# Kernel optimization log

Hardware: AMD Instinct MI355X
Metric: run time of the kernel (lower is better)

## Reference

```python
import jax, jax.numpy as jnp
import numpy as np

N = 8192        # total nodes in the batch of graphs
E = 262144      # edges (avg degree 32)
F_IN = 128      # input node features
G = 64          # graphs in batch
C = 10          # classes
K1, K2, K3 = 4096, 2048, 1024  # int(0.5*N), int(0.5*K1), int(0.5*K2)


def setup_inputs() -> dict:
    key = jax.random.key(0)
    ks = jax.random.split(key, 16)
    def lin(k, i, o):
        return jax.random.normal(k, (i, o), jnp.float32) / np.float32(np.sqrt(i))
    return {
        "x": jax.random.normal(ks[0], (N, F_IN), jnp.float32),
        "edge_index": jax.random.randint(ks[1], (2, E), 0, N),
        "batch": jnp.sort(jax.random.randint(ks[2], (N,), 0, G)),
        "W1": lin(ks[3], F_IN, 32), "b1": jnp.zeros((32,), jnp.float32),
        "W2": lin(ks[4], 32, 64),   "b2": jnp.zeros((64,), jnp.float32),
        "W3": lin(ks[5], 64, 128),  "b3": jnp.zeros((128,), jnp.float32),
        "W4": lin(ks[6], 128, 256), "b4": jnp.zeros((256,), jnp.float32),
        "W5": lin(ks[7], 384, 128), "b5": jnp.zeros((128,), jnp.float32),
        "W6": lin(ks[8], 192, 64),  "b6": jnp.zeros((64,), jnp.float32),
        "W7": lin(ks[9], 96, 32),   "b7": jnp.zeros((32,), jnp.float32),
        "p1": jax.random.normal(ks[10], (32,), jnp.float32),
        "p2": jax.random.normal(ks[11], (64,), jnp.float32),
        "p3": jax.random.normal(ks[12], (128,), jnp.float32),
        "Wl1": lin(ks[13], 64, 64),
        "Wc": lin(ks[14], 64, C), "bc": jnp.zeros((C,), jnp.float32),
    }


def _gcn(A, x, W, b):
    # PyG GCNConv (improved=False): out = D^-1/2 (A+I) D^-1/2 propagated src->dst.
    n = A.shape[0]
    Ah = A + jnp.eye(n, dtype=A.dtype)
    deg = Ah.sum(axis=0)                                  # degree at targets (cols)
    dinv = jnp.where(deg > 0, deg ** -0.5, 0.0).astype(A.dtype)
    An = dinv[:, None] * Ah * dinv[None, :]               # edge norm d[src]^-.5 * d[dst]^-.5
    return An.T @ (x @ W) + b                             # out[dst] += norm * (xW)[src]


def _gpool(A, x, p, k):
    # GPool: scores = Linear(x)/||p||, top-k select, gate by sigmoid, reindex dense adj.
    scores = (x @ p) / jnp.linalg.norm(p)                 # [n]
    vals, idx = jax.lax.top_k(scores, k)
    xp = x[idx] * jax.nn.sigmoid(vals)[:, None]
    Ap = (A[idx][:, idx] > 0).astype(x.dtype)             # dense_to_sparse rebinarizes
    return xp, Ap, idx


def reference(x, edge_index, batch, W1, b1, W2, b2, W3, b3, W4, b4, W5, b5,
              W6, b6, W7, b7, p1, p2, p3, Wl1, Wc, bc):
    elu = jax.nn.elu
    # to_dense_adj: dense N x N adjacency (duplicate edges accumulate)
    A = jnp.zeros((N, N), x.dtype).at[edge_index[0], edge_index[1]].add(1.0)
    x1 = elu(_gcn(A, x, W1, b1))
    x2, A2, i2 = _gpool(A, x1, p1, K1); x2 = elu(x2)
    x3 = elu(_gcn(A2, x2, W2, b2))
    x4, A4, i4 = _gpool(A2, x3, p2, K2); x4 = elu(x4)
    x5 = elu(_gcn(A4, x4, W3, b3))
    x6, A6, i6 = _gpool(A4, x5, p3, K3); x6 = elu(x6)
    x7 = elu(_gcn(A6, x6, W4, b4))
    u = jnp.zeros((K2, x7.shape[1]), x7.dtype).at[i6].set(x7)   # GUnpool
    x8 = elu(jnp.concatenate([u, x5], axis=1))
    x9 = elu(_gcn(A4, x8, W5, b5))
    u = jnp.zeros((K1, x9.shape[1]), x9.dtype).at[i4].set(x9)
    x10 = elu(jnp.concatenate([u, x3], axis=1))
    x11 = elu(_gcn(A2, x10, W6, b6))
    u = jnp.zeros((N, x11.shape[1]), x11.dtype).at[i2].set(x11)
    x12 = elu(jnp.concatenate([u, x1], axis=1))
    x13 = elu(_gcn(A, x12, W7, b7))
    gmax = jax.ops.segment_max(x13, batch, num_segments=G)      # global max pool
    gsum = jax.ops.segment_sum(x13, batch, num_segments=G)
    cnt = jax.ops.segment_sum(jnp.ones((N, 1), x13.dtype), batch, num_segments=G)
    h = elu(jnp.concatenate([gmax, gsum / cnt], axis=1))        # [G, 64]
    h = elu(h @ Wl1)
    return jax.nn.log_softmax(h @ Wc + bc, axis=-1)
```

## Files before the change

kernel.cpp:

```cpp
#include <hip/hip_runtime.h>
#include <math.h>

#define NN 8192
#define EE 262144
#define GG 64
#define CC 10
#define KK1 4096
#define KK2 2048
#define KK3 1024
#define PITCH 128

typedef unsigned long long ull;

__device__ __forceinline__ float eluf(float x) { return x > 0.f ? x : expm1f(x); }
__device__ __forceinline__ float sigf(float x) { return 1.f / (1.f + expf(-x)); }
__device__ __forceinline__ unsigned f2s(float f) {
    unsigned u = __float_as_uint(f);
    return (u & 0x80000000u) ? ~u : (u | 0x80000000u);
}

__global__ void k_init(const int* __restrict__ ei, int* __restrict__ cnt1,
                       int* __restrict__ csr1, const int* __restrict__ batch,
                       int* __restrict__ gstart, const float* __restrict__ X,
                       const float* __restrict__ W, float* __restrict__ Y) {
    __shared__ float Xs[32][33];
    __shared__ float Ws[32][36];
    int tid = threadIdx.x;
    if ((int)blockIdx.x >= 1024) {
        int txn = tid & 7, tym = tid >> 3;
        int m0 = ((int)blockIdx.x - 1024) * 32;
        float4 acc = make_float4(0.f, 0.f, 0.f, 0.f);
        for (int k0 = 0; k0 < 128; k0 += 32) {
            int r = tid >> 3, c4 = (tid & 7) << 2;
            *(float4*)&Xs[r][c4] = *(const float4*)&X[(size_t)(m0 + r) * 128 + k0 + c4];
            *(float4*)&Ws[r][c4] = *(const float4*)&W[(size_t)(k0 + r) * 32 + c4];
            __syncthreads();
#pragma unroll 8
            for (int kk = 0; kk < 32; kk++) {
                float4 wv = *(const float4*)&Ws[kk][txn * 4];
                float xv = Xs[tym][kk];
                acc.x += xv * wv.x; acc.y += xv * wv.y;
                acc.z += xv * wv.z; acc.w += xv * wv.w;
            }
            __syncthreads();
        }
        *(float4*)&Y[(size_t)(m0 + tym) * 32 + txn * 4] = acc;
        return;
    }
    int e = blockIdx.x * 256 + tid;
    int s = ei[e], d = ei[EE + e];
    int pos = atomicAdd(&cnt1[d], 1);
    csr1[(d << 7) + pos] = s;
    if (e < NN) {
        int g = batch[e];
        int prev = (e == 0) ? -1 : batch[e - 1];
        for (int gg = prev + 1; gg <= g; gg++) gstart[gg] = e;
        if (e == NN - 1)
            for (int gg = g + 1; gg <= GG; gg++) gstart[gg] = NN;
    }
}

template<int KPOOL, int F, int FOUT, int L1>
__global__ void k_pool_gemm_sub(const float* __restrict__ x, const float* __restrict__ score,
                                const int* __restrict__ idx, float* __restrict__ xW,
                                const float* __restrict__ W,
                                const int* __restrict__ csrP, const int* __restrict__ roffP,
                                const int* __restrict__ degP,
                                const int* __restrict__ invmap,
                                int* __restrict__ csrO, int* __restrict__ roffO,
                                int* __restrict__ degO, float* __restrict__ dinvO) {
    constexpr int MT = KPOOL / 32, NT = FOUT / 32, NPOOL = MT * NT;
    int tid = threadIdx.x;
    if ((int)blockIdx.x < NPOOL) {
        __shared__ float Xs[32][F + 4];
        __shared__ float Ws[32][36];
        __shared__ float sfac[32];
        __shared__ int sIdx[32];
        int mt = (int)blockIdx.x % MT, nt = (int)blockIdx.x / MT;
        int m0 = mt * 32, n0 = nt * 32;
        if (tid < 32) {
            int j = idx[m0 + tid];
            sIdx[tid] = j;
            sfac[tid] = sigf(score[j]);
        }
        __syncthreads();
        for (int i4 = tid; i4 < 32 * (F / 4); i4 += 256) {
            int r = i4 / (F / 4), c = i4 % (F / 4);
            float4 v = *(const float4*)&x[(size_t)sIdx[r] * F + c * 4];
            float sf = sfac[r];
            v.x = eluf(v.x * sf); v.y = eluf(v.y * sf);
            v.z = eluf(v.z * sf); v.w = eluf(v.w * sf);
            *(float4*)&Xs[r][c * 4] = v;
        }
        __syncthreads();
        int txn = tid & 7, tym = tid >> 3;
        float4 acc = make_float4(0.f, 0.f, 0.f, 0.f);
        for (int k0 = 0; k0 < F; k0 += 32) {
            {
                int r = tid >> 3, c4 = (tid & 7) << 2;
                *(float4*)&Ws[r][c4] = *(const float4*)&W[(size_t)(k0 + r) * FOUT + n0 + c4];
            }
            __syncthreads();
#pragma unroll 8
            for (int kk = 0; kk < 32; kk++) {
                float4 wv = *(const float4*)&Ws[kk][txn * 4];
                float xv = Xs[tym][k0 + kk];
                acc.x += xv * wv.x; acc.y += xv * wv.y;
                acc.z += xv * wv.z; acc.w += xv * wv.w;
            }
            __syncthreads();
        }
        *(float4*)&xW[(size_t)(m0 + tym) * FOUT + n0 + txn * 4] = acc;
        return;
    }
    int wid = (((int)blockIdx.x - NPOOL) * 256 + tid) >> 6;
    int lane = tid & 63;
    if (wid >= KPOOL) return;
    int j = idx[wid];
    int cnt = 0;
    if (L1) {
        int j0 = j << 7;
        int len = degP[j];
        int e0 = (lane < len) ? csrP[j0 + lane] : -1;
        int e1 = (64 + lane < len) ? csrP[j0 + 64 + lane] : -1;
        bool dup0 = false, dup1 = false;
        for (int q = 0; q < len - 1; q++) {
            int vq = (q < 64) ? __shfl(e0, q, 64) : __shfl(e1, q - 64, 64);
            if (lane > q && e0 == vq) dup0 = true;
            if (64 + lane > q && e1 == vq) dup1 = true;
        }
        {
            bool sel = (lane < len) && !dup0;
            int val = 0;
            if (sel) { int v = invmap[e0]; if (v > 0) val = v - 1; else sel = false; }
            ull m = __ballot(sel);
            if (sel) { int off = __popcll(m & ((1ull << lane) - 1ull)); csrO[j0 + cnt + off] = val; }
            cnt += __popcll(m);
        }
        {
            bool sel = (64 + lane < len) && !dup1;
            int val = 0;
            if (sel) { int v = invmap[e1]; if (v > 0) val = v - 1; else sel = false; }
            ull m = __ballot(sel);
            if (sel) { int off = __popcll(m & ((1ull << lane) - 1ull)); csrO[j0 + cnt + off] = val; }
            cnt += __popcll(m);
        }
        if (lane == 0) {
            roffO[wid] = j0;
            degO[wid] = cnt;
            dinvO[wid] = 1.f / sqrtf((float)(cnt + 1));
        }
    } else {
        int j0 = roffP[j];
        int len = degP[j];
        for (int base = 0; base < len; base += 64) {
            bool sel = false;
            int val = 0;
            if (base + lane < len) {
                int e = csrP[j0 + base + lane];
                int v = invmap[e];
                if (v > 0) { sel = true; val = v - 1; }
            }
            ull m = __ballot(sel);
            if (sel) { int off = __popcll(m & ((1ull << lane) - 1ull)); csrO[j0 + cnt + off] = val; }
            cnt += __popcll(m);
        }
        if (lane == 0) {
            roffO[wid] = j0;
            degO[wid] = cnt;
            dinvO[wid] = 1.f / sqrtf((float)(cnt + 1));
        }
    }
}

__global__ void k_gemm_up(const float* __restrict__ xl, const int* __restrict__ inv,
                          const float* __restrict__ xr, int Fl, int Fr,
                          const float* __restrict__ W, float* __restrict__ Y,
                          int M, int K, int F) {
    __shared__ float Xs[32][33];
    __shared__ float Ws[32][36];
    __shared__ int sIdx[32];
    int tid = threadIdx.x;
    int txn = tid & 7, tym = tid >> 3;
    int m0 = blockIdx.x * 32, n0 = blockIdx.y * 32;
    if (tid < 32) sIdx[tid] = inv[m0 + tid];
    float4 acc = make_float4(0.f, 0.f, 0.f, 0.f);
    __syncthreads();
    for (int k0 = 0; k0 < K; k0 += 32) {
        {
            int r = tid >> 3, c4 = (tid & 7) << 2;
            int kk = k0 + c4;
            float4 v;
            if (kk < Fl) {
                int rr = sIdx[r];
                v = (rr > 0) ? *(const float4*)&xl[(size_t)(rr - 1) * Fl + kk]
                             : make_float4(0.f, 0.f, 0.f, 0.f);
            } else {
                v = *(const float4*)&xr[(size_t)(m0 + r) * Fr + (kk - Fl)];
            }
            v.x = eluf(v.x); v.y = eluf(v.y); v.z = eluf(v.z); v.w = eluf(v.w);
            *(float4*)&Xs[r][c4] = v;
            *(float4*)&Ws[r][c4] = *(const float4*)&W[(size_t)(k0 + r) * F + n0 + c4];
        }
        __syncthreads();
#pragma unroll 8
        for (int kk = 0; kk < 32; kk++) {
            float4 wv = *(const float4*)&Ws[kk][txn * 4];
            float xv = Xs[tym][kk];
            acc.x += xv * wv.x; acc.y += xv * wv.y;
            acc.z += xv * wv.z; acc.w += xv * wv.w;
        }
        __syncthreads();
    }
    *(float4*)&Y[(size_t)(m0 + tym) * F + n0 + txn * 4] = acc;
}

template<int LOGF, int SCORE, int L1, int LS>
__global__ void k_prop(const int* __restrict__ csr, const int* __restrict__ roff,
                       const int* __restrict__ deg, const float* __restrict__ dinv,
                       const float* __restrict__ xW, const float* __restrict__ b,
                       float* __restrict__ xout, const float* __restrict__ p,
                       float* __restrict__ score) {
    constexpr int FQ = 1 << (LOGF - 2);
    constexpr int S = 1 << LS;
    constexpr int RL = FQ * S;
    const float4* xW4 = (const float4*)xW;
    int t = blockIdx.x * 256 + threadIdx.x;
    int d = t >> (LOGF - 2 + LS);
    int rem = t & (RL - 1);
    int q = rem >> LS, h = rem & (S - 1);
    int j0 = L1 ? (d << 7) : roff[d];
    int dg = deg[d];
    int j1 = j0 + dg;
    float dd = L1 ? (1.f / sqrtf((float)(dg + 1))) : dinv[d];
    int idx = (d << (LOGF - 2)) + q;
    float4 sum;
    if (h == 0) {
        float4 v0 = xW4[idx];
        sum = make_float4(dd * v0.x, dd * v0.y, dd * v0.z, dd * v0.w);
    } else {
        sum = make_float4(0.f, 0.f, 0.f, 0.f);
    }
    for (int j = j0 + h; j < j1; j += S) {
        int s = csr[j];
        float ds = L1 ? (1.f / sqrtf((float)(deg[s] + 1))) : dinv[s];
        float4 xv = xW4[(s << (LOGF - 2)) + q];
        sum.x += ds * xv.x; sum.y += ds * xv.y;
        sum.z += ds * xv.z; sum.w += ds * xv.w;
    }
#pragma unroll
    for (int m = 1; m < S; m <<= 1) {
        sum.x += __shfl_xor(sum.x, m, 64);
        sum.y += __shfl_xor(sum.y, m, 64);
        sum.z += __shfl_xor(sum.z, m, 64);
        sum.w += __shfl_xor(sum.w, m, 64);
    }
    float4 bv = *(const float4*)&b[q << 2];
    float4 o;
    o.x = eluf(dd * sum.x + bv.x);
    o.y = eluf(dd * sum.y + bv.y);
    o.z = eluf(dd * sum.z + bv.z);
    o.w = eluf(dd * sum.w + bv.w);
    if (h == 0) ((float4*)xout)[idx] = o;
    if (SCORE) {
        float4 pv = *(const float4*)&p[q << 2];
        float sc = 0.f, nr = 0.f;
        if (h == 0) {
            sc = o.x * pv.x + o.y * pv.y + o.z * pv.z + o.w * pv.w;
            nr = pv.x * pv.x + pv.y * pv.y + pv.z * pv.z + pv.w * pv.w;
        }
#pragma unroll
        for (int m = RL >> 1; m >= 1; m >>= 1) {
            sc += __shfl_xor(sc, m, 64);
            nr += __shfl_xor(nr, m, 64);
        }
        if (rem == 0) score[d] = sc / sqrtf(nr);
    }
}

__device__ __forceinline__ ull cex_shfl(ull v, int st, bool takeMax) {
    ull pv = __shfl_xor(v, st, 64);
    return takeMax ? (v > pv ? v : pv) : (v < pv ? v : pv);
}
__device__ __forceinline__ void cexr(ull& a, ull& b, bool desc) {
    if (desc ? (a < b) : (a > b)) { ull x = a; a = b; b = x; }
}

__global__ void k_wsort(const float* __restrict__ score, ull* __restrict__ keys,
                        int last, int k, int* __restrict__ out_idx,
                        int* __restrict__ invmap) {
    __shared__ ull sk[2048];
    int tid = threadIdx.x;
    int base = blockIdx.x << 11;
    int giA = base + tid, giB = giA + 1024;
    ull a = ((ull)f2s(score[giA]) << 32) | (unsigned)(~giA);
    ull b = ((ull)f2s(score[giB]) << 32) | (unsigned)(~giB);
    for (int sz = 2; sz <= 2048; sz <<= 1) {
        int st = sz >> 1;
        if (st >= 64) {
            sk[tid] = a; sk[tid + 1024] = b;
            __syncthreads();
            for (; st >= 64; st >>= 1) {
                int i = ((tid & ~(st - 1)) << 1) | (tid & (st - 1));
                int j = i | st;
                ull u = sk[i], v = sk[j];
                bool desc = (((base + i) & sz) == 0);
                if (desc ? (u < v) : (u > v)) { sk[i] = v; sk[j] = u; }
                __syncthreads();
            }
            a = sk[tid]; b = sk[tid + 1024];
        }
        for (; st >= 1; st >>= 1) {
            bool low = (tid & st) == 0;
            bool descA = ((giA & sz) == 0);
            bool descB = ((giB & sz) == 0);
            a = cex_shfl(a, st, descA == low);
            b = cex_shfl(b, st, descB == low);
        }
    }
    if (last) {
        if (giA < k) {
            int j = (int)(~(unsigned)(a & 0xFFFFFFFFu));
            out_idx[giA] = j; invmap[j] = giA + 1;
        }
        if (giB < k) {
            int j = (int)(~(unsigned)(b & 0xFFFFFFFFu));
            out_idx[giB] = j; invmap[j] = giB + 1;
        }
    } else {
        keys[giA] = a; keys[giB] = b;
    }
}

__global__ void k_stage4k_m(ull* __restrict__ keys) {
    __shared__ ull sk[4096];
    int tid = threadIdx.x;
    int base = blockIdx.x << 12;
    bool desc = ((base & 4096) == 0);
    ull k0 = keys[base + tid], k1 = keys[base + tid + 1024];
    ull k2 = keys[base + tid + 2048], k3 = keys[base + tid + 3072];
    cexr(k0, k2, desc); cexr(k1, k3, desc);
    sk[tid] = k0; sk[tid + 1024] = k1; sk[tid + 2048] = k2; sk[tid + 3072] = k3;
    __syncthreads();
    for (int st = 1024; st >= 64; st >>= 1) {
        for (int pp = tid; pp < 2048; pp += 1024) {
            int i = ((pp & ~(st - 1)) << 1) | (pp & (st - 1));
            int j = i | st;
            ull u = sk[i], v = sk[j];
            if (desc ? (u < v) : (u > v)) { sk[i] = v; sk[j] = u; }
        }
        __syncthreads();
    }
    k0 = sk[tid]; k1 = sk[tid + 1024]; k2 = sk[tid + 2048]; k3 = sk[tid + 3072];
    for (int st = 32; st >= 1; st >>= 1) {
        bool low = (tid & st) == 0;
        k0 = cex_shfl(k0, st, desc == low);
        k1 = cex_shfl(k1, st, desc == low);
        k2 = cex_shfl(k2, st, desc == low);
        k3 = cex_shfl(k3, st, desc == low);
    }
    keys[base + tid] = k0; keys[base + tid + 1024] = k1;
    keys[base + tid + 2048] = k2; keys[base + tid + 3072] = k3;
}

__global__ void k_stage8k_f(const ull* __restrict__ keys, int* __restrict__ out_idx,
                            int* __restrict__ invmap) {
    __shared__ ull sk[4096];
    int tid = threadIdx.x;
    ull a0 = keys[tid],        a1 = keys[tid + 1024];
    ull a2 = keys[tid + 2048], a3 = keys[tid + 3072];
    ull b0 = keys[tid + 4096], b1 = keys[tid + 5120];
    ull b2 = keys[tid + 6144], b3 = keys[tid + 7168];
    cexr(a0, b0, true); cexr(a1, b1, true);
    cexr(a2, b2, true); cexr(a3, b3, true);
    cexr(a0, a2, true); cexr(a1, a3, true);
    sk[tid] = a0; sk[tid + 1024] = a1; sk[tid + 2048] = a2; sk[tid + 3072] = a3;
    __syncthreads();
    for (int st = 1024; st >= 64; st >>= 1) {
        for (int pp = tid; pp < 2048; pp += 1024) {
            int i = ((pp & ~(st - 1)) << 1) | (pp & (st - 1));
            int j = i | st;
            ull u = sk[i], v = sk[j];
            if (u < v) { sk[i] = v; sk[j] = u; }
        }
        __syncthreads();
    }
    a0 = sk[tid]; a1 = sk[tid + 1024]; a2 = sk[tid + 2048]; a3 = sk[tid + 3072];
    for (int st = 32; st >= 1; st >>= 1) {
        bool low = (tid & st) == 0;
        a0 = cex_shfl(a0, st, low);
        a1 = cex_shfl(a1, st, low);
        a2 = cex_shfl(a2, st, low);
        a3 = cex_shfl(a3, st, low);
    }
    int p, j;
    p = tid;        j = (int)(~(unsigned)(a0 & 0xFFFFFFFFu)); out_idx[p] = j; invmap[j] = p + 1;
    p = tid + 1024; j = (int)(~(unsigned)(a1 & 0xFFFFFFFFu)); out_idx[p] = j; invmap[j] = p + 1;
    p = tid + 2048; j = (int)(~(unsigned)(a2 & 0xFFFFFFFFu)); out_idx[p] = j; invmap[j] = p + 1;
    p = tid + 3072; j = (int)(~(unsigned)(a3 & 0xFFFFFFFFu)); out_idx[p] = j; invmap[j] = p + 1;
}

__global__ void k_stage4k_f(const ull* __restrict__ keys, int* __restrict__ out_idx,
                            int* __restrict__ invmap) {
    __shared__ ull sk[2048];
    int tid = threadIdx.x;
    ull a0 = keys[tid],        a1 = keys[tid + 1024];
    ull a2 = keys[tid + 2048], a3 = keys[tid + 3072];
    cexr(a0, a2, true); cexr(a1, a3, true);
    sk[tid] = a0; sk[tid + 1024] = a1;
    __syncthreads();
    for (int st = 1024; st >= 64; st >>= 1) {
        int i = ((tid & ~(st - 1)) << 1) | (tid & (st - 1));
        int j = i | st;
        ull u = sk[i], v = sk[j];
        if (u < v) { sk[i] = v; sk[j] = u; }
        __syncthreads();
    }
    a0 = sk[tid]; a1 = sk[tid + 1024];
    for (int st = 32; st >= 1; st >>= 1) {
        bool low = (tid & st) == 0;
        a0 = cex_shfl(a0, st, low);
        a1 = cex_shfl(a1, st, low);
    }
    int p, j;
    p = tid;        j = (int)(~(unsigned)(a0 & 0xFFFFFFFFu)); out_idx[p] = j; invmap[j] = p + 1;
    p = tid + 1024; j = (int)(~(unsigned)(a1 & 0xFFFFFFFFu)); out_idx[p] = j; invmap[j] = p + 1;
}

__global__ void k_finale(const float* __restrict__ x13, const int* __restrict__ gstart,
                         const float* __restrict__ Wl1, const float* __restrict__ Wc,
                         const float* __restrict__ bc, float* __restrict__ out) {
    __shared__ float sm[8][32], ss[8][32];
    __shared__ float h0[64], h1[64], lg[CC];
    int g = blockIdx.x;
    int j0 = gstart[g], j1 = gstart[g + 1];
    int t = threadIdx.x;
    int f = t & 31, r = t >> 5;
    float m = -INFINITY, s = 0.f;
    for (int j = j0 + r; j < j1; j += 8) {
        float v = x13[(j << 5) + f];
        m = fmaxf(m, v);
        s += v;
    }
    sm[r][f] = m; ss[r][f] = s;
    __syncthreads();
    if (t < 32) {
        float mm = sm[0][t], sss = ss[0][t];
        for (int i = 1; i < 8; i++) { mm = fmaxf(mm, sm[i][t]); sss += ss[i][t]; }
        h0[t] = eluf(mm);
        h0[32 + t] = eluf(sss / (float)(j1 - j0));
    }
    __syncthreads();
    if (t < 64) {
        float sum = 0.f;
        for (int kk = 0; kk < 64; kk++) sum += h0[kk] * Wl1[kk * 64 + t];
        h1[t] = eluf(sum);
    }
    __syncthreads();
    if (t < CC) {
        float sum = bc[t];
        for (int kk = 0; kk < 64; kk++) sum += h1[kk] * Wc[kk * CC + t];
        lg[t] = sum;
    }
    __syncthreads();
    if (t == 0) {
        float mm = -1e30f;
        for (int c = 0; c < CC; c++) mm = fmaxf(mm, lg[c]);
        float se = 0.f;
        for (int c = 0; c < CC; c++) se += expf(lg[c] - mm);
        float lse = mm + logf(se);
        for (int c = 0; c < CC; c++) out[g * CC + c] = lg[c] - lse;
    }
}

static void run_topk(const float* score, ull* keys, int n, int k, int* out_idx,
                     int* invmap, hipStream_t stream) {
    if (n == 2048) {
        k_wsort<<<1, 1024, 0, stream>>>(score, keys, 1, k, out_idx, invmap);
    } else if (n == 4096) {
        k_wsort<<<2, 1024, 0, stream>>>(score, keys, 0, k, out_idx, invmap);
        k_stage4k_f<<<1, 1024, 0, stream>>>(keys, out_idx, invmap);
    } else {
        k_wsort<<<4, 1024, 0, stream>>>(score, keys, 0, k, out_idx, invmap);
        k_stage4k_m<<<2, 1024, 0, stream>>>(keys);
        k_stage8k_f<<<1, 1024, 0, stream>>>(keys, out_idx, invmap);
    }
}

extern "C" void kernel_launch(void* const* d_in, const int* in_sizes, int n_in,
                              void* d_out, int out_size, void* d_ws, size_t ws_size,
                              hipStream_t stream) {
    const float* x = (const float*)d_in[0];
    const int* ei = (const int*)d_in[1];
    const int* batch = (const int*)d_in[2];
    const float* W1 = (const float*)d_in[3];  const float* b1 = (const float*)d_in[4];
    const float* W2 = (const float*)d_in[5];  const float* b2 = (const float*)d_in[6];
    const float* W3 = (const float*)d_in[7];  const float* b3 = (const float*)d_in[8];
    const float* W4 = (const float*)d_in[9];  const float* b4 = (const float*)d_in[10];
    const float* W5 = (const float*)d_in[11]; const float* b5 = (const float*)d_in[12];
    const float* W6 = (const float*)d_in[13]; const float* b6 = (const float*)d_in[14];
    const float* W7 = (const float*)d_in[15]; const float* b7 = (const float*)d_in[16];
    const float* p1 = (const float*)d_in[17];
    const float* p2 = (const float*)d_in[18];
    const float* p3 = (const float*)d_in[19];
    const float* Wl1 = (const float*)d_in[20];
    const float* Wc = (const float*)d_in[21];
    const float* bc = (const float*)d_in[22];
    float* out = (float*)d_out;
    (void)in_sizes; (void)n_in; (void)out_size; (void)ws_size;

    char* w = (char*)d_ws;
    size_t off = 0;
    auto alloc = [&](size_t bytes) -> char* {
        char* p = w + off;
        off = (off + bytes + 255) & ~(size_t)255;
        return p;
    };

    size_t zero_begin = off;
    int* cnt1 = (int*)alloc(NN * 4);
    int* pos2 = (int*)alloc(NN * 4);
    int* inv4 = (int*)alloc(KK1 * 4);
    int* inv6 = (int*)alloc(KK2 * 4);
    size_t zero_len = off - zero_begin;

    float* dinv2 = (float*)alloc(KK1 * 4);
    float* dinv3 = (float*)alloc(KK2 * 4);
    float* dinv4 = (float*)alloc(KK3 * 4);
    int* roff2 = (int*)alloc(KK1 * 4); int* deg2 = (int*)alloc(KK1 * 4);
    int* roff3 = (int*)alloc(KK2 * 4); int* deg3 = (int*)alloc(KK2 * 4);
    int* roff4 = (int*)alloc(KK3 * 4); int* deg4 = (int*)alloc(KK3 * 4);
    int* csr1 = (int*)alloc((size_t)NN * PITCH * 4);
    int* csr2 = (int*)alloc((size_t)NN * PITCH * 4);
    int* csr3 = (int*)alloc((size_t)NN * PITCH * 4);
    int* csr4 = (int*)alloc((size_t)NN * PITCH * 4);
    float* xW = (float*)alloc((size_t)262144 * 4);
    float* x1 = (float*)alloc((size_t)NN * 32 * 4);
    float* x3 = (float*)alloc((size_t)KK1 * 64 * 4);
    float* x5 = (float*)alloc((size_t)KK2 * 128 * 4);
    float* x7 = (float*)alloc((size_t)KK3 * 256 * 4);
    float* x9 = (float*)alloc((size_t)KK2 * 128 * 4);
    float* x11 = (float*)alloc((size_t)KK1 * 64 * 4);
    float* x13 = (float*)alloc((size_t)NN * 32 * 4);
    float* score1 = (float*)alloc(NN * 4);
    float* score2 = (float*)alloc(KK1 * 4);
    float* score3 = (float*)alloc(KK2 * 4);
    int* i2 = (int*)alloc(KK1 * 4);
    int* i4 = (int*)alloc(KK2 * 4);
    int* i6 = (int*)alloc(KK3 * 4);
    ull* keys = (ull*)alloc((size_t)NN * 8);
    int* gstart = (int*)alloc((GG + 1) * 4);

    hipMemsetAsync(w + zero_begin, 0, zero_len, stream);

    const int B = 256;
    k_init<<<1280, B, 0, stream>>>(ei, cnt1, csr1, batch, gstart, x, W1, xW);

    k_prop<5, 1, 1, 3><<<2048, B, 0, stream>>>(csr1, nullptr, cnt1, nullptr, xW, b1,
                                               x1, p1, score1);

    run_topk(score1, keys, NN, KK1, i2, pos2, stream);
    k_pool_gemm_sub<KK1, 32, 64, 1><<<256 + KK1 / 4, B, 0, stream>>>(
        x1, score1, i2, xW, W2, csr1, nullptr, cnt1, pos2, csr2, roff2, deg2, dinv2);

    k_prop<6, 1, 0, 2><<<1024, B, 0, stream>>>(csr2, roff2, deg2, dinv2, xW, b2,
                                               x3, p2, score2);

    run_topk(score2, keys, KK1, KK2, i4, inv4, stream);
    k_pool_gemm_sub<KK2, 64, 128, 0><<<256 + KK2 / 4, B, 0, stream>>>(
        x3, score2, i4, xW, W3, csr2, roff2, deg2, inv4, csr3, roff3, deg3, dinv3);

    k_prop<7, 1, 0, 1><<<512, B, 0, stream>>>(csr3, roff3, deg3, dinv3, xW, b3,
                                              x5, p3, score3);

    run_topk(score3, keys, KK2, KK3, i6, inv6, stream);
    k_pool_gemm_sub<KK3, 128, 256, 0><<<256 + KK3 / 4, B, 0, stream>>>(
        x5, score3, i6, xW, W4, csr3, roff3, deg3, inv6, csr4, roff4, deg4, dinv4);

    k_prop<8, 0, 0, 1><<<512, B, 0, stream>>>(csr4, roff4, deg4, dinv4, xW, b4,
                                              x7, nullptr, nullptr);

    k_gemm_up<<<dim3(KK2 / 32, 4), B, 0, stream>>>(x7, inv6, x5, 256, 128,
                                                   W5, xW, KK2, 384, 128);
    k_prop<7, 0, 0, 2><<<1024, B, 0, stream>>>(csr3, roff3, deg3, dinv3, xW, b5,
                                               x9, nullptr, nullptr);

    k_gemm_up<<<dim3(KK1 / 32, 2), B, 0, stream>>>(x9, inv4, x3, 128, 64,
                                                   W6, xW, KK1, 192, 64);
    k_prop<6, 0, 0, 2><<<1024, B, 0, stream>>>(csr2, roff2, deg2, dinv2, xW, b6,
                                               x11, nullptr, nullptr);

    k_gemm_up<<<dim3(NN / 32, 1), B, 0, stream>>>(x11, pos2, x1, 64, 32,
                                                  W7, xW, NN, 96, 32);
    k_prop<5, 0, 1, 3><<<2048, B, 0, stream>>>(csr1, nullptr, cnt1, nullptr, xW, b7,
                                               x13, nullptr, nullptr);

    k_finale<<<GG, B, 0, stream>>>(x13, gstart, Wl1, Wc, bc, out);
}
```

Measured before the change: 312.8 us.

## Fuse multi-kernel bitonic top-k into one kernel with atomic-counter grid sync

Merges the separate bitonic sort stage kernels (local sort, 4k merge, 8k final merge) into a single launch per pooling level. Blocks signal completion through a zeroed global counter and spin-wait on it instead of relying on kernel boundaries. This removes three kernel launches and their inter-kernel gaps, but it depends on all blocks being co-resident and adds spin-wait cost.

```diff
diff --git a/kernel.cpp b/kernel.cpp
--- a/kernel.cpp
+++ b/kernel.cpp
@@ -286,145 +286,146 @@
     if (desc ? (a < b) : (a > b)) { ull x = a; a = b; b = x; }
 }
 
-__global__ void k_wsort(const float* __restrict__ score, ull* __restrict__ keys,
-                        int last, int k, int* __restrict__ out_idx,
-                        int* __restrict__ invmap) {
-    __shared__ ull sk[2048];
-    int tid = threadIdx.x;
-    int base = blockIdx.x << 11;
-    int giA = base + tid, giB = giA + 1024;
-    ull a = ((ull)f2s(score[giA]) << 32) | (unsigned)(~giA);
-    ull b = ((ull)f2s(score[giB]) << 32) | (unsigned)(~giB);
-    for (int sz = 2; sz <= 2048; sz <<= 1) {
-        int st = sz >> 1;
-        if (st >= 64) {
-            sk[tid] = a; sk[tid + 1024] = b;
-            __syncthreads();
-            for (; st >= 64; st >>= 1) {
-                int i = ((tid & ~(st - 1)) << 1) | (tid & (st - 1));
-                int j = i | st;
-                ull u = sk[i], v = sk[j];
-                bool desc = (((base + i) & sz) == 0);
-                if (desc ? (u < v) : (u > v)) { sk[i] = v; sk[j] = u; }
-                __syncthreads();
-            }
-            a = sk[tid]; b = sk[tid + 1024];
-        }
-        for (; st >= 1; st >>= 1) {
-            bool low = (tid & st) == 0;
-            bool descA = ((giA & sz) == 0);
-            bool descB = ((giB & sz) == 0);
-            a = cex_shfl(a, st, descA == low);
-            b = cex_shfl(b, st, descB == low);
-        }
-    }
-    if (last) {
-        if (giA < k) {
-            int j = (int)(~(unsigned)(a & 0xFFFFFFFFu));
-            out_idx[giA] = j; invmap[j] = giA + 1;
-        }
-        if (giB < k) {
-            int j = (int)(~(unsigned)(b & 0xFFFFFFFFu));
-            out_idx[giB] = j; invmap[j] = giB + 1;
-        }
-    } else {
-        keys[giA] = a; keys[giB] = b;
-    }
-}
-
-__global__ void k_stage4k_m(ull* __restrict__ keys) {
+__global__ void k_topk_f(const float* __restrict__ score, ull* __restrict__ keys,
+                         int N, int k, int* __restrict__ out_idx,
+                         int* __restrict__ invmap, int* __restrict__ ctr) {
     __shared__ ull sk[4096];
     int tid = threadIdx.x;
-    int base = blockIdx.x << 12;
-    bool desc = ((base & 4096) == 0);
-    ull k0 = keys[base + tid], k1 = keys[base + tid + 1024];
-    ull k2 = keys[base + tid + 2048], k3 = keys[base + tid + 3072];
-    cexr(k0, k2, desc); cexr(k1, k3, desc);
-    sk[tid] = k0; sk[tid + 1024] = k1; sk[tid + 2048] = k2; sk[tid + 3072] = k3;
-    __syncthreads();
-    for (int st = 1024; st >= 64; st >>= 1) {
-        for (int pp = tid; pp < 2048; pp += 1024) {
-            int i = ((pp & ~(st - 1)) << 1) | (pp & (st - 1));
-            int j = i | st;
-            ull u = sk[i], v = sk[j];
-            if (desc ? (u < v) : (u > v)) { sk[i] = v; sk[j] = u; }
-        }
-        __syncthreads();
-    }
-    k0 = sk[tid]; k1 = sk[tid + 1024]; k2 = sk[tid + 2048]; k3 = sk[tid + 3072];
-    for (int st = 32; st >= 1; st >>= 1) {
-        bool low = (tid & st) == 0;
-        k0 = cex_shfl(k0, st, desc == low);
-        k1 = cex_shfl(k1, st, desc == low);
-        k2 = cex_shfl(k2, st, desc == low);
-        k3 = cex_shfl(k3, st, desc == low);
-    }
-    keys[base + tid] = k0; keys[base + tid + 1024] = k1;
-    keys[base + tid + 2048] = k2; keys[base + tid + 3072] = k3;
-}
-
-__global__ void k_stage8k_f(const ull* __restrict__ keys, int* __restrict__ out_idx,
-                            int* __restrict__ invmap) {
-    __shared__ ull sk[4096];
-    int tid = threadIdx.x;
-    ull a0 = keys[tid],        a1 = keys[tid + 1024];
-    ull a2 = keys[tid + 2048], a3 = keys[tid + 3072];
-    ull b0 = keys[tid + 4096], b1 = keys[tid + 5120];
-    ull b2 = keys[tid + 6144], b3 = keys[tid + 7168];
-    cexr(a0, b0, true); cexr(a1, b1, true);
-    cexr(a2, b2, true); cexr(a3, b3, true);
-    cexr(a0, a2, true); cexr(a1, a3, true);
-    sk[tid] = a0; sk[tid + 1024] = a1; sk[tid + 2048] = a2; sk[tid + 3072] = a3;
-    __syncthreads();
-    for (int st = 1024; st >= 64; st >>= 1) {
-        for (int pp = tid; pp < 2048; pp += 1024) {
-            int i = ((pp & ~(st - 1)) << 1) | (pp & (st - 1));
+    int bid = blockIdx.x;
+    int nb = N >> 11;
+    {
+        int base = bid << 11;
+        int giA = base + tid, giB = giA + 1024;
+        ull a = ((ull)f2s(score[giA]) << 32) | (unsigned)(~giA);
+        ull b = ((ull)f2s(score[giB]) << 32) | (unsigned)(~giB);
+        for (int sz = 2; sz <= 2048; sz <<= 1) {
+            int st = sz >> 1;
+            if (st >= 64) {
+                sk[tid] = a; sk[tid + 1024] = b;
+                __syncthreads();
+                for (; st >= 64; st >>= 1) {
+                    int i = ((tid & ~(st - 1)) << 1) | (tid & (st - 1));
+                    int j = i | st;
+                    ull u = sk[i], v = sk[j];
+                    bool desc = (((base + i) & sz) == 0);
+                    if (desc ? (u < v) : (u > v)) { sk[i] = v; sk[j] = u; }
+                    __syncthreads();
+                }
+                a = sk[tid]; b = sk[tid + 1024];
+            }
+            for (; st >= 1; st >>= 1) {
+                bool low = (tid & st) == 0;
+                a = cex_shfl(a, st, ((giA & sz) == 0) == low);
+                b = cex_shfl(b, st, ((giB & sz) == 0) == low);
+            }
+        }
+        if (nb == 1) {
+            if (giA < k) { int j = (int)(~(unsigned)(a & 0xFFFFFFFFu)); out_idx[giA] = j; invmap[j] = giA + 1; }
+            if (giB < k) { int j = (int)(~(unsigned)(b & 0xFFFFFFFFu)); out_idx[giB] = j; invmap[j] = giB + 1; }
+            return;
+        }
+        keys[giA] = a; keys[giB] = b;
+    }
+    __syncthreads();
+    if (tid == 0) { __threadfence(); atomicAdd(ctr, 1); }
+
+    if (N == 4096) {
+        if (bid != 0) return;
+        if (tid == 0) { while (atomicAdd(ctr, 0) < 2) ; __threadfence(); }
+        __syncthreads();
+        ull a0 = keys[tid],        a1 = keys[tid + 1024];
+        ull a2 = keys[tid + 2048], a3 = keys[tid + 3072];
+        cexr(a0, a2, true); cexr(a1, a3, true);
+        sk[tid] = a0; sk[tid + 1024] = a1;
+        __syncthreads();
+        for (int st = 1024; st >= 64; st >>= 1) {
+            int i = ((tid & ~(st - 1)) << 1) | (tid & (st - 1));
             int j = i | st;
             ull u = sk[i], v = sk[j];
             if (u < v) { sk[i] = v; sk[j] = u; }
-        }
-        __syncthreads();
-    }
-    a0 = sk[tid]; a1 = sk[tid + 1024]; a2 = sk[tid + 2048]; a3 = sk[tid + 3072];
-    for (int st = 32; st >= 1; st >>= 1) {
-        bool low = (tid & st) == 0;
-        a0 = cex_shfl(a0, st, low);
-        a1 = cex_shfl(a1, st, low);
-        a2 = cex_shfl(a2, st, low);
-        a3 = cex_shfl(a3, st, low);
-    }
-    int p, j;
-    p = tid;        j = (int)(~(unsigned)(a0 & 0xFFFFFFFFu)); out_idx[p] = j; invmap[j] = p + 1;
-    p = tid + 1024; j = (int)(~(unsigned)(a1 & 0xFFFFFFFFu)); out_idx[p] = j; invmap[j] = p + 1;
-    p = tid + 2048; j = (int)(~(unsigned)(a2 & 0xFFFFFFFFu)); out_idx[p] = j; invmap[j] = p + 1;
-    p = tid + 3072; j = (int)(~(unsigned)(a3 & 0xFFFFFFFFu)); out_idx[p] = j; invmap[j] = p + 1;
-}
-
-__global__ void k_stage4k_f(const ull* __restrict__ keys, int* __restrict__ out_idx,
-                            int* __restrict__ invmap) {
-    __shared__ ull sk[2048];
-    int tid = threadIdx.x;
-    ull a0 = keys[tid],        a1 = keys[tid + 1024];
-    ull a2 = keys[tid + 2048], a3 = keys[tid + 3072];
-    cexr(a0, a2, true); cexr(a1, a3, true);
-    sk[tid] = a0; sk[tid + 1024] = a1;
-    __syncthreads();
-    for (int st = 1024; st >= 64; st >>= 1) {
-        int i = ((tid & ~(st - 1)) << 1) | (tid & (st - 1));
-        int j = i | st;
-        ull u = sk[i], v = sk[j];
-        if (u < v) { sk[i] = v; sk[j] = u; }
-        __syncthreads();
-    }
-    a0 = sk[tid]; a1 = sk[tid + 1024];
-    for (int st = 32; st >= 1; st >>= 1) {
-        bool low = (tid & st) == 0;
-        a0 = cex_shfl(a0, st, low);
-        a1 = cex_shfl(a1, st, low);
-    }
-    int p, j;
-    p = tid;        j = (int)(~(unsigned)(a0 & 0xFFFFFFFFu)); out_idx[p] = j; invmap[j] = p + 1;
-    p = tid + 1024; j = (int)(~(unsigned)(a1 & 0xFFFFFFFFu)); out_idx[p] = j; invmap[j] = p + 1;
+            __syncthreads();
+        }
+        a0 = sk[tid]; a1 = sk[tid + 1024];
+        for (int st = 32; st >= 1; st >>= 1) {
+            bool low = (tid & st) == 0;
+            a0 = cex_shfl(a0, st, low);
+            a1 = cex_shfl(a1, st, low);
+        }
+        int p, j;
+        p = tid;        j = (int)(~(unsigned)(a0 & 0xFFFFFFFFu)); out_idx[p] = j; invmap[j] = p + 1;
+        p = tid + 1024; j = (int)(~(unsigned)(a1 & 0xFFFFFFFFu)); out_idx[p] = j; invmap[j] = p + 1;
+        return;
+    }
+
+    if (bid >= 2) return;
+    if (tid == 0) { while (atomicAdd(ctr, 0) < 4) ; __threadfence(); }
+    __syncthreads();
+    {
+        int base = bid << 12;
+        bool desc = ((base & 4096) == 0);
+        ull k0 = keys[base + tid], k1 = keys[base + tid + 1024];
+        ull k2 = keys[base + tid + 2048], k3 = keys[base + tid + 3072];
+        cexr(k0, k2, desc); cexr(k1, k3, desc);
+        sk[tid] = k0; sk[tid + 1024] = k1; sk[tid + 2048] = k2; sk[tid + 3072] = k3;
+        __syncthreads();
+        for (int st = 1024; st >= 64; st >>= 1) {
+            for (int pp = tid; pp < 2048; pp += 1024) {
+                int i = ((pp & ~(st - 1)) << 1) | (pp & (st - 1));
+                int j = i | st;
+                ull u = sk[i], v = sk[j];
+                if (desc ? (u < v) : (u > v)) { sk[i] = v; sk[j] = u; }
+            }
+            __syncthreads();
+        }
+        k0 = sk[tid]; k1 = sk[tid + 1024]; k2 = sk[tid + 2048]; k3 = sk[tid + 3072];
+        for (int st = 32; st >= 1; st >>= 1) {
+            bool low = (tid & st) == 0;
+            k0 = cex_shfl(k0, st, desc == low);
+            k1 = cex_shfl(k1, st, desc == low);
+            k2 = cex_shfl(k2, st, desc == low);
+            k3 = cex_shfl(k3, st, desc == low);
+        }
+        keys[base + tid] = k0; keys[base + tid + 1024] = k1;
+        keys[base + tid + 2048] = k2; keys[base + tid + 3072] = k3;
+    }
+    __syncthreads();
+    if (tid == 0) { __threadfence(); atomicAdd(ctr, 1); }
+    if (bid != 0) return;
+    if (tid == 0) { while (atomicAdd(ctr, 0) < 6) ; __threadfence(); }
+    __syncthreads();
+    {
+        ull a0 = keys[tid],        a1 = keys[tid + 1024];
+        ull a2 = keys[tid + 2048], a3 = keys[tid + 3072];
+        ull b0 = keys[tid + 4096], b1 = keys[tid + 5120];
+        ull b2 = keys[tid + 6144], b3 = keys[tid + 7168];
+        cexr(a0, b0, true); cexr(a1, b1, true);
+        cexr(a2, b2, true); cexr(a3, b3, true);
+        cexr(a0, a2, true); cexr(a1, a3, true);
+        sk[tid] = a0; sk[tid + 1024] = a1; sk[tid + 2048] = a2; sk[tid + 3072] = a3;
+        __syncthreads();
+        for (int st = 1024; st >= 64; st >>= 1) {
+            for (int pp = tid; pp < 2048; pp += 1024) {
+                int i = ((pp & ~(st - 1)) << 1) | (pp & (st - 1));
+                int j = i | st;
+                ull u = sk[i], v = sk[j];
+                if (u < v) { sk[i] = v; sk[j] = u; }
+            }
+            __syncthreads();
+        }
+        a0 = sk[tid]; a1 = sk[tid + 1024]; a2 = sk[tid + 2048]; a3 = sk[tid + 3072];
+        for (int st = 32; st >= 1; st >>= 1) {
+            bool low = (tid & st) == 0;
+            a0 = cex_shfl(a0, st, low);
+            a1 = cex_shfl(a1, st, low);
+            a2 = cex_shfl(a2, st, low);
+            a3 = cex_shfl(a3, st, low);
+        }
+        int p, j;
+        p = tid;        j = (int)(~(unsigned)(a0 & 0xFFFFFFFFu)); out_idx[p] = j; invmap[j] = p + 1;
+        p = tid + 1024; j = (int)(~(unsigned)(a1 & 0xFFFFFFFFu)); out_idx[p] = j; invmap[j] = p + 1;
+        p = tid + 2048; j = (int)(~(unsigned)(a2 & 0xFFFFFFFFu)); out_idx[p] = j; invmap[j] = p + 1;
+        p = tid + 3072; j = (int)(~(unsigned)(a3 & 0xFFFFFFFFu)); out_idx[p] = j; invmap[j] = p + 1;
+    }
 }
 
 __global__ void k_finale(const float* __restrict__ x13, const int* __restrict__ gstart,
@@ -470,20 +471,6 @@
         for (int c = 0; c < CC; c++) se += expf(lg[c] - mm);
         float lse = mm + logf(se);
         for (int c = 0; c < CC; c++) out[g * CC + c] = lg[c] - lse;
-    }
-}
-
-static void run_topk(const float* score, ull* keys, int n, int k, int* out_idx,
-                     int* invmap, hipStream_t stream) {
-    if (n == 2048) {
-        k_wsort<<<1, 1024, 0, stream>>>(score, keys, 1, k, out_idx, invmap);
-    } else if (n == 4096) {
-        k_wsort<<<2, 1024, 0, stream>>>(score, keys, 0, k, out_idx, invmap);
-        k_stage4k_f<<<1, 1024, 0, stream>>>(keys, out_idx, invmap);
-    } else {
-        k_wsort<<<4, 1024, 0, stream>>>(score, keys, 0, k, out_idx, invmap);
-        k_stage4k_m<<<2, 1024, 0, stream>>>(keys);
-        k_stage8k_f<<<1, 1024, 0, stream>>>(keys, out_idx, invmap);
     }
 }
 
@@ -522,6 +509,7 @@
     int* pos2 = (int*)alloc(NN * 4);
     int* inv4 = (int*)alloc(KK1 * 4);
     int* inv6 = (int*)alloc(KK2 * 4);
+    int* tkctr = (int*)alloc(2 * 4);
     size_t zero_len = off - zero_begin;
 
     float* dinv2 = (float*)alloc(KK1 * 4);
@@ -559,21 +547,21 @@
     k_prop<5, 1, 1, 3><<<2048, B, 0, stream>>>(csr1, nullptr, cnt1, nullptr, xW, b1,
                                                x1, p1, score1);
 
-    run_topk(score1, keys, NN, KK1, i2, pos2, stream);
+    k_topk_f<<<4, 1024, 0, stream>>>(score1, keys, NN, KK1, i2, pos2, tkctr);
     k_pool_gemm_sub<KK1, 32, 64, 1><<<256 + KK1 / 4, B, 0, stream>>>(
         x1, score1, i2, xW, W2, csr1, nullptr, cnt1, pos2, csr2, roff2, deg2, dinv2);
 
     k_prop<6, 1, 0, 2><<<1024, B, 0, stream>>>(csr2, roff2, deg2, dinv2, xW, b2,
                                                x3, p2, score2);
 
-    run_topk(score2, keys, KK1, KK2, i4, inv4, stream);
+    k_topk_f<<<2, 1024, 0, stream>>>(score2, keys, KK1, KK2, i4, inv4, tkctr + 1);
     k_pool_gemm_sub<KK2, 64, 128, 0><<<256 + KK2 / 4, B, 0, stream>>>(
         x3, score2, i4, xW, W3, csr2, roff2, deg2, inv4, csr3, roff3, deg3, dinv3);
 
     k_prop<7, 1, 0, 1><<<512, B, 0, stream>>>(csr3, roff3, deg3, dinv3, xW, b3,
                                               x5, p3, score3);
 
-    run_topk(score3, keys, KK2, KK3, i6, inv6, stream);
+    k_topk_f<<<1, 1024, 0, stream>>>(score3, keys, KK2, KK3, i6, inv6, nullptr);
     k_pool_gemm_sub<KK3, 128, 256, 0><<<256 + KK3 / 4, B, 0, stream>>>(
         x5, score3, i6, xW, W4, csr3, roff3, deg3, inv6, csr4, roff4, deg4, dinv4);
 
```

After: 310.3 us (median of 2 runs). Within noise of the previous version (-0.8%).
